# Performance work log

Measured on AMD Instinct MI355X. Metric: run time of the kernel, lower is better.

Reference implementation:

```python
import jax, jax.numpy as jnp
import numpy as np

N_NODES = 100000


def setup_inputs() -> dict:
    key = jax.random.key(0)
    k1, k2, k3, k4 = jax.random.split(key, 4)
    E = 1600000
    in_dim, out_dim = 256, 64
    h = jax.random.normal(k1, (N_NODES, in_dim), dtype=jnp.float32)
    src = jax.random.randint(k2, (E,), 0, N_NODES, dtype=jnp.int64)
    dst = jax.random.randint(k3, (E,), 0, N_NODES, dtype=jnp.int64)
    W = jax.random.normal(k4, (in_dim, out_dim), dtype=jnp.float32) * (1.0 / np.sqrt(in_dim))
    b = jnp.zeros((out_dim,), dtype=jnp.float32)
    return {"h": h, "src": src, "dst": dst, "W": W, "b": b}


def reference(h, src, dst, W, b):
    # dgl GraphConv, norm='both': out = D_in^{-1/2} A D_out^{-1/2} h W + b
    E = src.shape[0]
    ones = jnp.ones((E,), dtype=h.dtype)
    deg_out = jax.ops.segment_sum(ones, src, num_segments=N_NODES)  # out-degree of src nodes
    deg_in = jax.ops.segment_sum(ones, dst, num_segments=N_NODES)   # in-degree of dst nodes
    norm_src = jnp.clip(deg_out, 1.0, None) ** -0.5                  # [N]
    norm_dst = jnp.clip(deg_in, 1.0, None) ** -0.5                   # [N]
    # in_dim > out_dim: project first (as dgl does), then aggregate small features
    x = (h * norm_src[:, None]) @ W                                  # [N, out_dim]
    msgs = x[src]                                                    # [E, out_dim] gather
    agg = jax.ops.segment_sum(msgs, dst, num_segments=N_NODES)      # [N, out_dim] scatter-add
    out = agg * norm_dst[:, None] + b
    # ReLU; dropout is identity in eval mode
    return jax.nn.relu(out)
```

## Files before the change

### kernel.cpp

```cpp
#include <hip/hip_runtime.h>
#include <hip/hip_fp16.h>

#define N_NODES 100000
#define IN_DIM 256
#define OUT_DIM 64
#define NT 782
#define NB 256
#define SCHUNK 4096
#define SB ((NT * NB + SCHUNK - 1) / SCHUNK)
#define SCAN_M (NT * NB)

typedef _Float16 half8 __attribute__((ext_vector_type(8)));
typedef float f32x4 __attribute__((ext_vector_type(4)));

__global__ __launch_bounds__(256) void count_kernel(const int* __restrict__ src,
                                                    const int* __restrict__ dst,
                                                    int* __restrict__ CD, int* __restrict__ CS,
                                                    int E, int chunk) {
    __shared__ int hd[NT], hs[NT];
    const int t = threadIdx.x, blk = blockIdx.x;
    for (int i = t; i < NT; i += 256) { hd[i] = 0; hs[i] = 0; }
    __syncthreads();
    const int lo = blk * chunk;
    int hi = lo + chunk; if (hi > E) hi = E;
    for (int i = lo + t; i < hi; i += 256) {
        atomicAdd(&hd[dst[i] >> 7], 1);
        atomicAdd(&hs[src[i] >> 7], 1);
    }
    __syncthreads();
    for (int i = t; i < NT; i += 256) {
        CD[i * NB + blk] = hd[i];
        CS[i * NB + blk] = hs[i];
    }
}

__global__ __launch_bounds__(256) void scan_blocks_kernel(int* __restrict__ CD, int* __restrict__ CS,
                                                          int* __restrict__ BSD, int* __restrict__ BSS) {
    int cid = blockIdx.x;
    int* arr; int* bs;
    if (cid < SB) { arr = CD; bs = BSD; } else { arr = CS; bs = BSS; cid -= SB; }
    const int t = threadIdx.x;
    const int base = cid * SCHUNK + t * 16;
    int pre[16];
    int s = 0;
#pragma unroll
    for (int r = 0; r < 16; ++r) {
        int v = (base + r < SCAN_M) ? arr[base + r] : 0;
        pre[r] = s; s += v;
    }
    const int lane = t & 63;
    int incl = s;
#pragma unroll
    for (int off = 1; off < 64; off <<= 1) {
        int y = __shfl_up(incl, off);
        if (lane >= off) incl += y;
    }
    int wave_excl = incl - s;
    __shared__ int wtot[4];
    if (lane == 63) wtot[t >> 6] = incl;
    __syncthreads();
    int woff = 0;
    for (int w = 0; w < (t >> 6); ++w) woff += wtot[w];
    int bexcl = woff + wave_excl;
#pragma unroll
    for (int r = 0; r < 16; ++r)
        if (base + r < SCAN_M) arr[base + r] = bexcl + pre[r];
    if (t == 0) bs[cid] = wtot[0] + wtot[1] + wtot[2] + wtot[3];
}

__global__ void scan_sums_kernel(int* __restrict__ BSD, int* __restrict__ BSS) {
    const int t = threadIdx.x;
    const int lane = t & 63;
    int* bs = (t < 64) ? BSD : BSS;
    int v = (lane < SB) ? bs[lane] : 0;
    int incl = v;
#pragma unroll
    for (int off = 1; off < 64; off <<= 1) {
        int y = __shfl_up(incl, off);
        if (lane >= off) incl += y;
    }
    if (lane < SB) bs[lane] = incl - v;
}

__global__ __launch_bounds__(256) void scatter_kernel(const int* __restrict__ src,
                                                      const int* __restrict__ dst,
                                                      const int* __restrict__ CD, const int* __restrict__ CS,
                                                      const int* __restrict__ BSD, const int* __restrict__ BSS,
                                                      int* __restrict__ binnedD,
                                                      unsigned char* __restrict__ srcb,
                                                      int E, int chunk) {
    __shared__ int curD[NT], curS[NT];
    const int t = threadIdx.x, blk = blockIdx.x;
    for (int i = t; i < NT; i += 256) {
        int idx = i * NB + blk;
        curD[i] = CD[idx] + BSD[idx >> 12];
        curS[i] = CS[idx] + BSS[idx >> 12];
    }
    __syncthreads();
    const int lo = blk * chunk;
    int hi = lo + chunk; if (hi > E) hi = E;
    for (int i = lo + t; i < hi; i += 256) {
        int s = src[i], d = dst[i];
        int p = atomicAdd(&curD[d >> 7], 1);
        binnedD[p] = (s << 7) | (d & 127);
        int ps = atomicAdd(&curS[s >> 7], 1);
        srcb[ps] = (unsigned char)(s & 127);
    }
}

__global__ __launch_bounds__(256) void tile_kernel(const int* __restrict__ CD, const int* __restrict__ CS,
                                                   const int* __restrict__ BSD, const int* __restrict__ BSS,
                                                   const int* __restrict__ binnedD,
                                                   const unsigned char* __restrict__ srcb,
                                                   int* __restrict__ csr,
                                                   int* __restrict__ offs, int* __restrict__ cnt,
                                                   int* __restrict__ deg_out, int E) {
    __shared__ int h[128], cur[128];
    __shared__ int w0tot;
    const int bin = blockIdx.x, t = threadIdx.x, lane = t & 63;
    const int i0 = bin * NB;

    if (t < 128) h[t] = 0;
    __syncthreads();
    const int base = CD[i0] + BSD[i0 >> 12];
    const int next = (bin + 1 < NT) ? (CD[i0 + NB] + BSD[(i0 + NB) >> 12]) : E;
    const int m = next - base;
    for (int k = t; k < m; k += 256) atomicAdd(&h[binnedD[base + k] & 127], 1);
    __syncthreads();
    int v = (t < 128) ? h[t] : 0;
    int incl = v;
#pragma unroll
    for (int off = 1; off < 64; off <<= 1) {
        int y = __shfl_up(incl, off);
        if (lane >= off) incl += y;
    }
    if (t == 63) w0tot = incl;
    __syncthreads();
    int excl = incl - v + ((t >= 64 && t < 128) ? w0tot : 0);
    if (t < 128) {
        cur[t] = excl;
        int node = bin * 128 + t;
        if (node < N_NODES) { offs[node] = base + excl; cnt[node] = v; }
    }
    __syncthreads();
    for (int k = t; k < m; k += 256) {
        int rec = binnedD[base + k];
        int p = atomicAdd(&cur[rec & 127], 1);
        csr[base + p] = rec >> 7;
    }

    __syncthreads();
    if (t < 128) h[t] = 0;
    __syncthreads();
    const int sb = CS[i0] + BSS[i0 >> 12];
    const int sn = (bin + 1 < NT) ? (CS[i0 + NB] + BSS[(i0 + NB) >> 12]) : E;
    const int sm = sn - sb;
    for (int k = t; k < sm; k += 256) atomicAdd(&h[srcb[sb + k]], 1);
    __syncthreads();
    if (t < 128) {
        int node = bin * 128 + t;
        if (node < N_NODES) deg_out[node] = h[t];
    }
}

#define A_LD 136
__global__ __launch_bounds__(256) void gemm_kernel(const float* __restrict__ hmat,
                                                   const float* __restrict__ W,
                                                   const int* __restrict__ deg_out,
                                                   __half* __restrict__ xh) {
    __shared__ _Float16 sA[64 * A_LD];
    __shared__ _Float16 sB[64 * A_LD];
    const int t = threadIdx.x;
    const int lane = t & 63;
    const int w = t >> 6;
    const int row0 = blockIdx.x * 64;
    const int m0 = (w & 1) * 32;
    const int n0 = (w >> 1) * 32;

    f32x4 acc00 = {0.f, 0.f, 0.f, 0.f}, acc01 = {0.f, 0.f, 0.f, 0.f};
    f32x4 acc10 = {0.f, 0.f, 0.f, 0.f}, acc11 = {0.f, 0.f, 0.f, 0.f};

    for (int khalf = 0; khalf < 2; ++khalf) {
        const int k0 = khalf * 128;
        __syncthreads();
#pragma unroll
        for (int it = 0; it < 8; ++it) {
            int f = t + it * 256;
            int row = f >> 5;
            int c4 = f & 31;
            int grow = row0 + row; if (grow >= N_NODES) grow = N_NODES - 1;
            float4 v = *(const float4*)(hmat + (size_t)grow * IN_DIM + k0 + c4 * 4);
            _Float16 p[4];
            p[0] = (_Float16)v.x; p[1] = (_Float16)v.y;
            p[2] = (_Float16)v.z; p[3] = (_Float16)v.w;
            *(uint2*)&sA[row * A_LD + c4 * 4] = *(uint2*)p;
        }
        {
            int n = t & 63;
            int kk0 = (t >> 6) * 32;
#pragma unroll
            for (int kb = 0; kb < 8; ++kb) {
                _Float16 p[4];
#pragma unroll
                for (int u = 0; u < 4; ++u)
                    p[u] = (_Float16)W[(size_t)(k0 + kk0 + kb * 4 + u) * OUT_DIM + n];
                *(uint2*)&sB[n * A_LD + kk0 + kb * 4] = *(uint2*)p;
            }
        }
        __syncthreads();
#pragma unroll
        for (int kb = 0; kb < 4; ++kb) {
            int koff = kb * 32 + (lane >> 4) * 8;
            half8 a0 = *(const half8*)&sA[(m0 + (lane & 15)) * A_LD + koff];
            half8 a1 = *(const half8*)&sA[(m0 + 16 + (lane & 15)) * A_LD + koff];
            half8 b0 = *(const half8*)&sB[(n0 + (lane & 15)) * A_LD + koff];
            half8 b1 = *(const half8*)&sB[(n0 + 16 + (lane & 15)) * A_LD + koff];
            acc00 = __builtin_amdgcn_mfma_f32_16x16x32_f16(a0, b0, acc00, 0, 0, 0);
            acc01 = __builtin_amdgcn_mfma_f32_16x16x32_f16(a0, b1, acc01, 0, 0, 0);
            acc10 = __builtin_amdgcn_mfma_f32_16x16x32_f16(a1, b0, acc10, 0, 0, 0);
            acc11 = __builtin_amdgcn_mfma_f32_16x16x32_f16(a1, b1, acc11, 0, 0, 0);
        }
    }

    const int col16 = lane & 15;
    const int rq = (lane >> 4) * 4;
#pragma unroll
    for (int mi = 0; mi < 2; ++mi) {
        float nrm[4];
#pragma unroll
        for (int r = 0; r < 4; ++r) {
            int row = row0 + m0 + mi * 16 + rq + r;
            int d = (row < N_NODES) ? deg_out[row] : 1;
            nrm[r] = rsqrtf((float)(d < 1 ? 1 : d));
        }
#pragma unroll
        for (int ni = 0; ni < 2; ++ni) {
            const f32x4 a = (mi == 0) ? (ni == 0 ? acc00 : acc01)
                                      : (ni == 0 ? acc10 : acc11);
            int col = n0 + ni * 16 + col16;
#pragma unroll
            for (int r = 0; r < 4; ++r) {
                int row = row0 + m0 + mi * 16 + rq + r;
                if (row < N_NODES)
                    xh[(size_t)row * OUT_DIM + col] = __float2half(a[r] * nrm[r]);
            }
        }
    }
}

__global__ __launch_bounds__(256) void aggregate_kernel(const int* __restrict__ offs,
                                                        const int* __restrict__ cnt,
                                                        const int* __restrict__ csr,
                                                        const __half* __restrict__ xh,
                                                        const float* __restrict__ b,
                                                        float* __restrict__ out) {
    const int t = threadIdx.x;
    const int lane = t & 63;
    const int wid = t >> 6;
    const int node = blockIdx.x * 4 + wid;
    const int g = lane >> 3;
    const int c = lane & 7;

    const int start = offs[node];
    const int n = cnt[node];

    float acc[8] = {0.f, 0.f, 0.f, 0.f, 0.f, 0.f, 0.f, 0.f};
    for (int base = 0; base < n; base += 64) {
        int k = base + lane;
        int sidx = (k < n) ? csr[start + k] : 0;
        int m = n - base; if (m > 64) m = 64;
        for (int rb = 0; rb < m; rb += 32) {
            uint4 raw[4]; float wq[4];
#pragma unroll
            for (int q = 0; q < 4; ++q) {
                int e = rb + 8 * q + g;
                int s = __shfl(sidx, e);
                bool val = e < m;
                s = val ? s : 0;
                wq[q] = val ? 1.f : 0.f;
                raw[q] = *(const uint4*)(xh + (size_t)s * OUT_DIM + 8 * c);
            }
#pragma unroll
            for (int q = 0; q < 4; ++q) {
                const __half2* hp = (const __half2*)&raw[q];
#pragma unroll
                for (int p = 0; p < 4; ++p) {
                    float2 f = __half22float2(hp[p]);
                    acc[2 * p]     = fmaf(wq[q], f.x, acc[2 * p]);
                    acc[2 * p + 1] = fmaf(wq[q], f.y, acc[2 * p + 1]);
                }
            }
        }
    }

#pragma unroll
    for (int off = 8; off < 64; off <<= 1) {
#pragma unroll
        for (int p = 0; p < 8; ++p)
            acc[p] += __shfl_xor(acc[p], off);
    }

    if (g == 0) {
        float nrm = rsqrtf((float)(n < 1 ? 1 : n));
        float4 bv0 = *(const float4*)&b[c * 8];
        float4 bv1 = *(const float4*)&b[c * 8 + 4];
        float4 r0, r1;
        r0.x = fmaxf(fmaf(acc[0], nrm, bv0.x), 0.f);
        r0.y = fmaxf(fmaf(acc[1], nrm, bv0.y), 0.f);
        r0.z = fmaxf(fmaf(acc[2], nrm, bv0.z), 0.f);
        r0.w = fmaxf(fmaf(acc[3], nrm, bv0.w), 0.f);
        r1.x = fmaxf(fmaf(acc[4], nrm, bv1.x), 0.f);
        r1.y = fmaxf(fmaf(acc[5], nrm, bv1.y), 0.f);
        r1.z = fmaxf(fmaf(acc[6], nrm, bv1.z), 0.f);
        r1.w = fmaxf(fmaf(acc[7], nrm, bv1.w), 0.f);
        float4* orow = (float4*)(out + (size_t)node * OUT_DIM + c * 8);
        orow[0] = r0;
        orow[1] = r1;
    }
}

extern "C" void kernel_launch(void* const* d_in, const int* in_sizes, int n_in,
                              void* d_out, int out_size, void* d_ws, size_t ws_size,
                              hipStream_t stream) {
    const float* h   = (const float*)d_in[0];
    const int*   src = (const int*)d_in[1];
    const int*   dst = (const int*)d_in[2];
    const float* W   = (const float*)d_in[3];
    const float* b   = (const float*)d_in[4];
    float* out = (float*)d_out;
    const int E = in_sizes[1];
    const int chunk = (E + NB - 1) / NB;

    char* ws = (char*)d_ws;
    int*           CD      = (int*)(ws);
    int*           CS      = (int*)(ws + 800768);
    int*           BSD     = (int*)(ws + 1601536);
    int*           BSS     = (int*)(ws + 1601792);
    int*           binnedD = (int*)(ws + 1602048);
    unsigned char* srcb    = (unsigned char*)(ws + 8002048);
    int*           csr     = (int*)(ws + 9602048);
    int*           offs    = (int*)(ws + 16002048);
    int*           cntA    = (int*)(ws + 16402048);
    int*           deg_out = (int*)(ws + 16802048);
    __half*        xh      = (__half*)(ws + 17202048);

    count_kernel<<<NB, 256, 0, stream>>>(src, dst, CD, CS, E, chunk);
    scan_blocks_kernel<<<2 * SB, 256, 0, stream>>>(CD, CS, BSD, BSS);
    scan_sums_kernel<<<1, 128, 0, stream>>>(BSD, BSS);
    scatter_kernel<<<NB, 256, 0, stream>>>(src, dst, CD, CS, BSD, BSS, binnedD, srcb, E, chunk);
    tile_kernel<<<NT, 256, 0, stream>>>(CD, CS, BSD, BSS, binnedD, srcb, csr, offs, cntA, deg_out, E);
    gemm_kernel<<<(N_NODES + 63) / 64, 256, 0, stream>>>(h, W, deg_out, xh);
    aggregate_kernel<<<N_NODES / 4, 256, 0, stream>>>(offs, cntA, csr, xh, b, out);
}
```

Baseline: 295.3 us.

## Fold chunk-sum scan into consumers and stream GEMM A operand from global

```diff
diff --git a/kernel.cpp b/kernel.cpp
--- a/kernel.cpp
+++ b/kernel.cpp
@@ -68,18 +68,22 @@
     if (t == 0) bs[cid] = wtot[0] + wtot[1] + wtot[2] + wtot[3];
 }
 
-__global__ void scan_sums_kernel(int* __restrict__ BSD, int* __restrict__ BSS) {
-    const int t = threadIdx.x;
-    const int lane = t & 63;
-    int* bs = (t < 64) ? BSD : BSS;
-    int v = (lane < SB) ? bs[lane] : 0;
-    int incl = v;
-#pragma unroll
-    for (int off = 1; off < 64; off <<= 1) {
-        int y = __shfl_up(incl, off);
-        if (lane >= off) incl += y;
-    }
-    if (lane < SB) bs[lane] = incl - v;
+__device__ __forceinline__ void scan_chunk_sums(const int* __restrict__ BSD,
+                                                const int* __restrict__ BSS,
+                                                int* sBSD, int* sBSS, int t) {
+    if (t < 128) {
+        const int lane = t & 63;
+        const int* bs = (t < 64) ? BSD : BSS;
+        int* sb = (t < 64) ? sBSD : sBSS;
+        int v = (lane < SB) ? bs[lane] : 0;
+        int incl = v;
+#pragma unroll
+        for (int off = 1; off < 64; off <<= 1) {
+            int y = __shfl_up(incl, off);
+            if (lane >= off) incl += y;
+        }
+        if (lane < SB) sb[lane] = incl - v;
+    }
 }
 
 __global__ __launch_bounds__(256) void scatter_kernel(const int* __restrict__ src,
@@ -90,11 +94,14 @@
                                                       unsigned char* __restrict__ srcb,
                                                       int E, int chunk) {
     __shared__ int curD[NT], curS[NT];
+    __shared__ int sBSD[SB], sBSS[SB];
     const int t = threadIdx.x, blk = blockIdx.x;
+    scan_chunk_sums(BSD, BSS, sBSD, sBSS, t);
+    __syncthreads();
     for (int i = t; i < NT; i += 256) {
         int idx = i * NB + blk;
-        curD[i] = CD[idx] + BSD[idx >> 12];
-        curS[i] = CS[idx] + BSS[idx >> 12];
+        curD[i] = CD[idx] + sBSD[idx >> 12];
+        curS[i] = CS[idx] + sBSS[idx >> 12];
     }
     __syncthreads();
     const int lo = blk * chunk;
@@ -117,13 +124,16 @@
                                                    int* __restrict__ deg_out, int E) {
     __shared__ int h[128], cur[128];
     __shared__ int w0tot;
+    __shared__ int sBSD[SB], sBSS[SB];
     const int bin = blockIdx.x, t = threadIdx.x, lane = t & 63;
     const int i0 = bin * NB;
 
+    scan_chunk_sums(BSD, BSS, sBSD, sBSS, t);
     if (t < 128) h[t] = 0;
     __syncthreads();
-    const int base = CD[i0] + BSD[i0 >> 12];
-    const int next = (bin + 1 < NT) ? (CD[i0 + NB] + BSD[(i0 + NB) >> 12]) : E;
+
+    const int base = CD[i0] + sBSD[i0 >> 12];
+    const int next = (bin + 1 < NT) ? (CD[i0 + NB] + sBSD[(i0 + NB) >> 12]) : E;
     const int m = next - base;
     for (int k = t; k < m; k += 256) atomicAdd(&h[binnedD[base + k] & 127], 1);
     __syncthreads();
@@ -152,8 +162,8 @@
     __syncthreads();
     if (t < 128) h[t] = 0;
     __syncthreads();
-    const int sb = CS[i0] + BSS[i0 >> 12];
-    const int sn = (bin + 1 < NT) ? (CS[i0 + NB] + BSS[(i0 + NB) >> 12]) : E;
+    const int sb = CS[i0] + sBSS[i0 >> 12];
+    const int sn = (bin + 1 < NT) ? (CS[i0 + NB] + sBSS[(i0 + NB) >> 12]) : E;
     const int sm = sn - sb;
     for (int k = t; k < sm; k += 256) atomicAdd(&h[srcb[sb + k]], 1);
     __syncthreads();
@@ -163,87 +173,71 @@
     }
 }
 
-#define A_LD 136
+#define B_LD 264
 __global__ __launch_bounds__(256) void gemm_kernel(const float* __restrict__ hmat,
                                                    const float* __restrict__ W,
                                                    const int* __restrict__ deg_out,
                                                    __half* __restrict__ xh) {
-    __shared__ _Float16 sA[64 * A_LD];
-    __shared__ _Float16 sB[64 * A_LD];
+    __shared__ _Float16 sB[64 * B_LD];
     const int t = threadIdx.x;
     const int lane = t & 63;
     const int w = t >> 6;
     const int row0 = blockIdx.x * 64;
-    const int m0 = (w & 1) * 32;
-    const int n0 = (w >> 1) * 32;
-
-    f32x4 acc00 = {0.f, 0.f, 0.f, 0.f}, acc01 = {0.f, 0.f, 0.f, 0.f};
-    f32x4 acc10 = {0.f, 0.f, 0.f, 0.f}, acc11 = {0.f, 0.f, 0.f, 0.f};
-
-    for (int khalf = 0; khalf < 2; ++khalf) {
-        const int k0 = khalf * 128;
-        __syncthreads();
-#pragma unroll
-        for (int it = 0; it < 8; ++it) {
-            int f = t + it * 256;
-            int row = f >> 5;
-            int c4 = f & 31;
-            int grow = row0 + row; if (grow >= N_NODES) grow = N_NODES - 1;
-            float4 v = *(const float4*)(hmat + (size_t)grow * IN_DIM + k0 + c4 * 4);
-            _Float16 p[4];
-            p[0] = (_Float16)v.x; p[1] = (_Float16)v.y;
-            p[2] = (_Float16)v.z; p[3] = (_Float16)v.w;
-            *(uint2*)&sA[row * A_LD + c4 * 4] = *(uint2*)p;
+
+#pragma unroll
+    for (int it = 0; it < 16; ++it) {
+        int f = t + it * 256;
+        int k = f >> 4;
+        int n4 = (f & 15) * 4;
+        float4 v = *(const float4*)(W + (size_t)k * OUT_DIM + n4);
+        sB[(n4 + 0) * B_LD + k] = (_Float16)v.x;
+        sB[(n4 + 1) * B_LD + k] = (_Float16)v.y;
+        sB[(n4 + 2) * B_LD + k] = (_Float16)v.z;
+        sB[(n4 + 3) * B_LD + k] = (_Float16)v.w;
+    }
+    __syncthreads();
+
+    const int m16 = lane & 15;
+    const int kq = lane >> 4;
+    int grow = row0 + w * 16 + m16;
+    const float* arow = hmat + (size_t)(grow < N_NODES ? grow : N_NODES - 1) * IN_DIM;
+
+    f32x4 acc[4] = {{0.f,0.f,0.f,0.f},{0.f,0.f,0.f,0.f},{0.f,0.f,0.f,0.f},{0.f,0.f,0.f,0.f}};
+
+#pragma unroll
+    for (int kb = 0; kb < 8; ++kb) {
+        const int koff = kb * 32 + kq * 8;
+        float4 alo = *(const float4*)(arow + koff);
+        float4 ahi = *(const float4*)(arow + koff + 4);
+        _Float16 af[8];
+        af[0] = (_Float16)alo.x; af[1] = (_Float16)alo.y;
+        af[2] = (_Float16)alo.z; af[3] = (_Float16)alo.w;
+        af[4] = (_Float16)ahi.x; af[5] = (_Float16)ahi.y;
+        af[6] = (_Float16)ahi.z; af[7] = (_Float16)ahi.w;
+        half8 a = *(half8*)af;
+#pragma unroll
+        for (int ni = 0; ni < 4; ++ni) {
+            half8 b = *(const half8*)&sB[(ni * 16 + m16) * B_LD + koff];
+            acc[ni] = __builtin_amdgcn_mfma_f32_16x16x32_f16(a, b, acc[ni], 0, 0, 0);
         }
-        {
-            int n = t & 63;
-            int kk0 = (t >> 6) * 32;
-#pragma unroll
-            for (int kb = 0; kb < 8; ++kb) {
-                _Float16 p[4];
-#pragma unroll
-                for (int u = 0; u < 4; ++u)
-                    p[u] = (_Float16)W[(size_t)(k0 + kk0 + kb * 4 + u) * OUT_DIM + n];
-                *(uint2*)&sB[n * A_LD + kk0 + kb * 4] = *(uint2*)p;
-            }
-        }
-        __syncthreads();
-#pragma unroll
-        for (int kb = 0; kb < 4; ++kb) {
-            int koff = kb * 32 + (lane >> 4) * 8;
-            half8 a0 = *(const half8*)&sA[(m0 + (lane & 15)) * A_LD + koff];
-            half8 a1 = *(const half8*)&sA[(m0 + 16 + (lane & 15)) * A_LD + koff];
-            half8 b0 = *(const half8*)&sB[(n0 + (lane & 15)) * A_LD + koff];
-            half8 b1 = *(const half8*)&sB[(n0 + 16 + (lane & 15)) * A_LD + koff];
-            acc00 = __builtin_amdgcn_mfma_f32_16x16x32_f16(a0, b0, acc00, 0, 0, 0);
-            acc01 = __builtin_amdgcn_mfma_f32_16x16x32_f16(a0, b1, acc01, 0, 0, 0);
-            acc10 = __builtin_amdgcn_mfma_f32_16x16x32_f16(a1, b0, acc10, 0, 0, 0);
-            acc11 = __builtin_amdgcn_mfma_f32_16x16x32_f16(a1, b1, acc11, 0, 0, 0);
-        }
-    }
-
-    const int col16 = lane & 15;
-    const int rq = (lane >> 4) * 4;
-#pragma unroll
-    for (int mi = 0; mi < 2; ++mi) {
-        float nrm[4];
+    }
+
+    const int rq = kq * 4;
+    float nrm[4];
+#pragma unroll
+    for (int r = 0; r < 4; ++r) {
+        int row = row0 + w * 16 + rq + r;
+        int d = (row < N_NODES) ? deg_out[row] : 1;
+        nrm[r] = rsqrtf((float)(d < 1 ? 1 : d));
+    }
+#pragma unroll
+    for (int ni = 0; ni < 4; ++ni) {
+        int col = ni * 16 + m16;
 #pragma unroll
         for (int r = 0; r < 4; ++r) {
-            int row = row0 + m0 + mi * 16 + rq + r;
-            int d = (row < N_NODES) ? deg_out[row] : 1;
-            nrm[r] = rsqrtf((float)(d < 1 ? 1 : d));
-        }
-#pragma unroll
-        for (int ni = 0; ni < 2; ++ni) {
-            const f32x4 a = (mi == 0) ? (ni == 0 ? acc00 : acc01)
-                                      : (ni == 0 ? acc10 : acc11);
-            int col = n0 + ni * 16 + col16;
-#pragma unroll
-            for (int r = 0; r < 4; ++r) {
-                int row = row0 + m0 + mi * 16 + rq + r;
-                if (row < N_NODES)
-                    xh[(size_t)row * OUT_DIM + col] = __float2half(a[r] * nrm[r]);
-            }
+            int row = row0 + w * 16 + rq + r;
+            if (row < N_NODES)
+                xh[(size_t)row * OUT_DIM + col] = __float2half(acc[ni][r] * nrm[r]);
         }
     }
 }
@@ -346,7 +340,6 @@
 
     count_kernel<<<NB, 256, 0, stream>>>(src, dst, CD, CS, E, chunk);
     scan_blocks_kernel<<<2 * SB, 256, 0, stream>>>(CD, CS, BSD, BSS);
-    scan_sums_kernel<<<1, 128, 0, stream>>>(BSD, BSS);
     scatter_kernel<<<NB, 256, 0, stream>>>(src, dst, CD, CS, BSD, BSS, binnedD, srcb, E, chunk);
     tile_kernel<<<NT, 256, 0, stream>>>(CD, CS, BSD, BSS, binnedD, srcb, csr, offs, cntA, deg_out, E);
     gemm_kernel<<<(N_NODES + 63) / 64, 256, 0, stream>>>(h, W, deg_out, xh);
```

Result: no change. 299.7 us (+1.5%).
